# Kernel optimization log

Measured on AMD Instinct MI355X. Metric: run time of the kernel, lower is better.

Reference implementation:

```python
import jax, jax.numpy as jnp
import numpy as np

NUM_SAMPLES = 4096
TAU = 0.07
EPS = 1e-20


def setup_inputs() -> dict:
    key = jax.random.key(0)
    flows = jax.random.normal(key, (32, 2, 512, 512), dtype=jnp.float32)
    return {"flows": flows}


def reference(flows):
    # flows: [b, 2, h, w]
    b, _, h, w = flows.shape
    hw = h * w
    # sampling weights: L2 norm over the 2 flow components, scaled by 1/tau
    dist = jnp.sqrt(jnp.sum(flows * flows, axis=1)) / TAU  # [b, h, w]
    dist = dist.reshape(b, hw)  # [b, h*w]
    # torch.multinomial(dist, k) without replacement == Gumbel-top-k on log-weights
    logits = jnp.log(dist + EPS)
    g = jax.random.gumbel(jax.random.key(42), (b, hw), dtype=flows.dtype)
    _, indices = jax.lax.top_k(logits + g, NUM_SAMPLES)  # [b, num_samples] int32
    # scatter-based mask (equivalent to one_hot(indices).max(dim=1), without the
    # huge [b, num_samples, h*w] intermediate)
    batch_idx = jnp.arange(b)[:, None]  # [b, 1]
    flat_masks = jnp.zeros((b, hw), dtype=flows.dtype).at[batch_idx, indices].set(1.0)
    masks = flat_masks.reshape(b, 1, h, w)  # [b, 1, h, w]
    sparse_output = masks * flows  # [b, 2, h, w]
    sparse_output = jnp.concatenate([sparse_output, masks], axis=1)  # [b, 3, h, w]
    return sparse_output, indices, masks
```

## Files before the change

### kernel.cpp

```cpp
#include <hip/hip_runtime.h>
#include <stdint.h>

#define HW 262144
#define NB 32
#define TOPK 4096
#define NTOTAL (NB * HW)
#define GBLK 4096
#define CBLK 32768

#define OUT_F4 8421376u
#define GTHREADS 524288u

typedef float f32x4 __attribute__((ext_vector_type(4)));

#define OFF_WIN 33554432
#define OFF_HA  35651584
#define OFF_HB  37748736
#define OFF_STA 39845888
#define OFF_STT 39846144
#define OFF_FLG 39846272
#define OFF_CNT 39846400

__device__ __forceinline__ uint32_t rotl32(uint32_t x, int d) {
  return (x << d) | (x >> (32 - d));
}

__device__ __forceinline__ void threefry2x32_k42(uint32_t x0, uint32_t x1,
                                                 uint32_t& o0, uint32_t& o1) {
  const uint32_t ks0 = 0u;
  const uint32_t ks1 = 42u;
  const uint32_t ks2 = 0x1BD11BDAu ^ 0u ^ 42u;
  x0 += ks0;
  x1 += ks1;
#define TF_ROUND(r) { x0 += x1; x1 = rotl32(x1, (r)); x1 ^= x0; }
  TF_ROUND(13) TF_ROUND(15) TF_ROUND(26) TF_ROUND(6)
  x0 += ks1; x1 += ks2 + 1u;
  TF_ROUND(17) TF_ROUND(29) TF_ROUND(16) TF_ROUND(24)
  x0 += ks2; x1 += ks0 + 2u;
  TF_ROUND(13) TF_ROUND(15) TF_ROUND(26) TF_ROUND(6)
  x0 += ks0; x1 += ks1 + 3u;
  TF_ROUND(17) TF_ROUND(29) TF_ROUND(16) TF_ROUND(24)
  x0 += ks1; x1 += ks2 + 4u;
  TF_ROUND(13) TF_ROUND(15) TF_ROUND(26) TF_ROUND(6)
  x0 += ks2; x1 += ks0 + 5u;
#undef TF_ROUND
  o0 = x0;
  o1 = x1;
}

__device__ __forceinline__ float eigen_plogf(float xin) {
#pragma clang fp contract(off)
  uint32_t ux = __float_as_uint(xin);
  int e_int = (int)(ux >> 23) - 126;
  float x = __uint_as_float((ux & 0x007fffffu) | 0x3f000000u);
  float e = (float)e_int;
  const float SQRTHF = 0.707106781186547524f;
  bool m = (x < SQRTHF);
  float tmp = m ? x : 0.0f;
  x = x - 1.0f;
  e = e - (m ? 1.0f : 0.0f);
  x = x + tmp;
  float x2 = x * x;
  float x3 = x2 * x;
  float y  = fmaf(7.0376836292e-2f,  x, -1.1514610310e-1f);
  float y1 = fmaf(-1.2420140846e-1f, x,  1.4249322787e-1f);
  float y2 = fmaf(2.0000714765e-1f,  x, -2.4999993993e-1f);
  y  = fmaf(y,  x,  1.1676998740e-1f);
  y1 = fmaf(y1, x, -1.6668057665e-1f);
  y2 = fmaf(y2, x,  3.3333331174e-1f);
  y  = fmaf(y,  x3, y1);
  y  = fmaf(y,  x3, y2);
  y  = y * x3;
  float ey1 = e * -2.12194440e-4f;
  float t2  = x2 * 0.5f;
  y = y + ey1;
  x = x - t2;
  float ey2 = e * 0.693359375f;
  x = x + y;
  x = x + ey2;
  return x;
}

__device__ __forceinline__ float np_logf(float xin) {
#pragma clang fp contract(off)
  uint32_t ux = __float_as_uint(xin);
  int e2 = (int)(ux >> 23) - 127;
  float mant = __uint_as_float((ux & 0x007fffffu) | 0x3f800000u);
  if (mant >= 1.5f) { mant = mant * 0.5f; e2 += 1; }
  float e = (float)e2;
  float t = mant - 1.0f;
  float num = fmaf(2.589979117907922693523e-02f, t, 3.808837741388407920751e-01f);
  num = fmaf(num, t, 1.480000633400055983228e+00f);
  num = fmaf(num, t, 2.112677543073053063722e+00f);
  num = fmaf(num, t, 9.999999999999998702752e-01f);
  num = num * t;
  float den = fmaf(5.875095403124574342950e-03f, t, 1.546476374983906719538e-01f);
  den = fmaf(den, t, 9.864942958519418960339e-01f);
  den = fmaf(den, t, 2.453006071784736363091e+00f);
  den = fmaf(den, t, 2.612677543073109236779e+00f);
  den = fmaf(den, t, 1.0f);
  float r = num / den;
  return fmaf(e, 0.693147182464599609375f, r);
}

__device__ __forceinline__ uint32_t order_key(const float* __restrict__ flows,
                                              int p, uint32_t bits) {
#pragma clang fp contract(off)
  int b = p >> 18;
  int j = p & (HW - 1);
  const float* fb = flows + ((size_t)b << 19);
  float x = fb[j];
  float y = fb[j + HW];
  float xx = x * x;
  float yy = y * y;
  float ss = xx + yy;
  float sq = (float)sqrt((double)ss);
  float dist = (float)((double)sq / (double)0.07f);
  float logits = np_logf(dist + 1e-20f);
  float f = __uint_as_float((bits >> 9) | 0x3f800000u) - 1.0f;
  float u = fmaxf(f, 1.17549435e-38f);
  float g = -eigen_plogf(-eigen_plogf(u));
  float s = logits + g;
  uint32_t mm = __float_as_uint(s);
  mm = (mm & 0x80000000u) ? ~mm : (mm | 0x80000000u);
  return ~mm;
}

__global__ __launch_bounds__(1024) void k_compute(const float* __restrict__ flows,
                                                  uint32_t* __restrict__ d,
                                                  uint32_t* __restrict__ histA) {
  __shared__ uint32_t lh[16384];
  for (int i = threadIdx.x; i < 16384; i += 1024) lh[i] = 0u;
  __syncthreads();
  int base = blockIdx.x * CBLK;
  int b = base >> 18;
  for (int it = 0; it < CBLK / 1024; ++it) {
    int p = base + it * 1024 + threadIdx.x;
    uint32_t o0, o1;
    threefry2x32_k42(0u, (uint32_t)p, o0, o1);
    uint32_t dv = order_key(flows, p, o0 ^ o1);
    d[p] = dv;
    atomicAdd(&lh[dv >> 18], 1u);
  }
  __syncthreads();
  uint32_t* hb = histA + ((uint32_t)b << 14);
  for (int i = threadIdx.x; i < 16384; i += 1024) {
    uint32_t c = lh[i];
    if (c) atomicAdd(&hb[i], c);
  }
}

__global__ __launch_bounds__(1024) void k_scanAB(const uint32_t* __restrict__ histA,
                                                 const uint32_t* __restrict__ d,
                                                 uint32_t* __restrict__ histB,
                                                 uint32_t* __restrict__ stateA,
                                                 uint32_t* __restrict__ stateT,
                                                 uint32_t* __restrict__ flag) {
  __shared__ uint32_t ls[1024];
  __shared__ uint32_t bc[3];
  int b = blockIdx.x;
  {
    const uint32_t* h = histA + ((uint32_t)b << 14);
    int base = threadIdx.x * 16;
    uint32_t s = 0;
    for (int i = 0; i < 16; ++i) s += h[base + i];
    ls[threadIdx.x] = s;
    __syncthreads();
    for (int off = 1; off < 1024; off <<= 1) {
      uint32_t v = (threadIdx.x >= off) ? ls[threadIdx.x - off] : 0u;
      __syncthreads();
      ls[threadIdx.x] += v;
      __syncthreads();
    }
    uint32_t incl = ls[threadIdx.x];
    uint32_t excl = incl - s;
    if (excl < TOPK && TOPK <= incl) {
      uint32_t cum = excl;
      for (int i = 0; i < 16; ++i) {
        uint32_t c = h[base + i];
        if (cum + c >= TOPK) {
          uint32_t B = (uint32_t)(base + i);
          stateA[2 * b] = B;
          stateA[2 * b + 1] = TOPK - cum;
          stateT[b] = (B << 18) | 0x3FFFFu;
          uint32_t ov = (cum + c > 8192u) ? 1u : 0u;
          flag[b] = ov;
          bc[0] = B; bc[1] = TOPK - cum; bc[2] = ov;
          break;
        }
        cum += c;
      }
    }
  }
  __syncthreads();
  if (bc[2] == 0u) return;
  uint32_t B = bc[0];
  uint32_t target = bc[1];
  uint32_t* h2 = histB + ((uint32_t)b << 14);
  const uint32_t* db = d + ((size_t)b << 18);
  for (int it = 0; it < HW / 1024; ++it) {
    uint32_t dv = db[it * 1024 + threadIdx.x];
    if ((dv >> 18) == B)
      atomicAdd(&h2[(dv >> 4) & 0x3FFFu], 1u);
  }
  __threadfence();
  __syncthreads();
  {
    int base = threadIdx.x * 16;
    uint32_t s = 0;
    for (int i = 0; i < 16; ++i) s += h2[base + i];
    ls[threadIdx.x] = s;
    __syncthreads();
    for (int off = 1; off < 1024; off <<= 1) {
      uint32_t v = (threadIdx.x >= off) ? ls[threadIdx.x - off] : 0u;
      __syncthreads();
      ls[threadIdx.x] += v;
      __syncthreads();
    }
    uint32_t incl = ls[threadIdx.x];
    uint32_t excl = incl - s;
    if (excl < target && target <= incl) {
      uint32_t cum = excl;
      for (int i = 0; i < 16; ++i) {
        uint32_t c = h2[base + i];
        if (cum + c >= target) {
          stateT[b] = (B << 18) | ((uint32_t)(base + i) << 4) | 0xFu;
          break;
        }
        cum += c;
      }
    }
  }
}

__global__ __launch_bounds__(256) void k_gather(const uint32_t* __restrict__ d,
                                                const uint32_t* __restrict__ stateT,
                                                uint32_t* __restrict__ cnt,
                                                unsigned long long* __restrict__ winners,
                                                f32x4* __restrict__ outz) {
  __shared__ unsigned long long buf[GBLK];
  __shared__ uint32_t lcnt;
  __shared__ uint32_t gbase;
  int base = blockIdx.x * GBLK;
  int b = base >> 18;
  uint32_t T = stateT[b];
  uint32_t gt = (uint32_t)blockIdx.x * 256u + threadIdx.x;
  const f32x4 z4 = {0.f, 0.f, 0.f, 0.f};
  if (threadIdx.x == 0) lcnt = 0u;
  __syncthreads();
  for (int it = 0; it < GBLK / 256; ++it) {
    int p = base + it * 256 + threadIdx.x;
    uint32_t dv = d[p];
    outz[(uint32_t)it * GTHREADS + gt] = z4;
    if (dv <= T) {
      uint32_t pos = atomicAdd(&lcnt, 1u);
      buf[pos] = ((unsigned long long)dv << 32) |
                 (unsigned long long)(p & (HW - 1));
    }
  }
  { uint32_t z = 16u * GTHREADS + gt;
    if (z < OUT_F4) outz[z] = z4; }
  __syncthreads();
  uint32_t n = lcnt;
  if (threadIdx.x == 0 && n) gbase = atomicAdd(&cnt[b], n);
  __syncthreads();
  for (uint32_t i = threadIdx.x; i < n; i += 256) {
    uint32_t pos = gbase + i;
    if (pos < 8192u) winners[(size_t)b * 8192 + pos] = buf[i];
  }
}

__global__ __launch_bounds__(1024) void k_sort1(const uint32_t* __restrict__ cnt,
                                                unsigned long long* __restrict__ winners) {
  __shared__ unsigned long long s[1024];
  int blk = blockIdx.x;
  int b = blk >> 3;
  int c = blk & 7;
  uint32_t n = cnt[b];
  if (n > 8192u) n = 8192u;
  int goff = b * 8192 + c * 1024;
  int t = threadIdx.x;
  s[t] = ((uint32_t)(c * 1024 + t) < n) ? winners[goff + t]
                                        : 0xFFFFFFFFFFFFFFFFull;
  __syncthreads();
  for (int k = 2; k <= 1024; k <<= 1) {
    for (int j = k >> 1; j > 0; j >>= 1) {
      int ixj = t ^ j;
      if (ixj > t) {
        bool up = ((t & k) == 0);
        unsigned long long a = s[t];
        unsigned long long cc = s[ixj];
        if ((a > cc) == up) { s[t] = cc; s[ixj] = a; }
      }
      __syncthreads();
    }
  }
  winners[goff + t] = s[t];
}

__global__ __launch_bounds__(1024) void k_rank(const unsigned long long* __restrict__ winners,
                                               const float* __restrict__ flows,
                                               float* __restrict__ out0,
                                               float* __restrict__ out_idx,
                                               float* __restrict__ out_masks) {
  __shared__ unsigned long long s[8192];
  int b = blockIdx.x >> 3;
  int part = blockIdx.x & 7;
  for (int i = threadIdx.x; i < 8192; i += 1024)
    s[i] = winners[(size_t)b * 8192 + i];
  __syncthreads();
  const float* fb = flows + ((size_t)b << 19);
  int i = (part << 10) + threadIdx.x;
  unsigned long long w = s[i];
  if (w != 0xFFFFFFFFFFFFFFFFull) {
    int rank = threadIdx.x;
    for (int c = 0; c < 8; ++c) {
      if (c == part) continue;
      int lo = 0, hi = 1024;
      while (lo < hi) {
        int mid = (lo + hi) >> 1;
        if (s[(c << 10) + mid] < w) lo = mid + 1; else hi = mid;
      }
      rank += lo;
    }
    if (rank < TOPK) {
      uint32_t idx = (uint32_t)(w & 0xFFFFFFFFull);
      out_idx[(size_t)b * TOPK + rank] = (float)idx;
      float x = fb[idx];
      float y = fb[idx + HW];
      size_t o = ((size_t)b * 3) * HW + idx;
      out0[o] = x;
      out0[o + HW] = y;
      out0[o + 2 * HW] = 1.0f;
      out_masks[(size_t)b * HW + idx] = 1.0f;
    }
  }
}

extern "C" void kernel_launch(void* const* d_in, const int* in_sizes, int n_in,
                              void* d_out, int out_size, void* d_ws, size_t ws_size,
                              hipStream_t stream) {
  const float* flows = (const float*)d_in[0];
  float* out = (float*)d_out;
  char* ws = (char*)d_ws;

  uint32_t* d = (uint32_t*)ws;
  unsigned long long* winners = (unsigned long long*)(ws + OFF_WIN);
  uint32_t* histA = (uint32_t*)(ws + OFF_HA);
  uint32_t* histB = (uint32_t*)(ws + OFF_HB);
  uint32_t* stateA = (uint32_t*)(ws + OFF_STA);
  uint32_t* stateT = (uint32_t*)(ws + OFF_STT);
  uint32_t* flag = (uint32_t*)(ws + OFF_FLG);
  uint32_t* cnt = (uint32_t*)(ws + OFF_CNT);

  float* out_idx = out + (size_t)NB * 3 * HW;
  float* out_masks = out_idx + (size_t)NB * TOPK;

  (void)hipMemsetAsync(ws + OFF_HA, 0, 4194304 + 1024, stream);

  k_compute<<<NTOTAL / CBLK, 1024, 0, stream>>>(flows, d, histA);
  k_scanAB<<<NB, 1024, 0, stream>>>(histA, d, histB, stateA, stateT, flag);
  k_gather<<<NTOTAL / GBLK, 256, 0, stream>>>(d, stateT, cnt, winners,
                                              (f32x4*)out);
  k_sort1<<<NB * 8, 1024, 0, stream>>>(cnt, winners);
  k_rank<<<NB * 8, 1024, 0, stream>>>(winners, flows, out, out_idx, out_masks);
}
```

Baseline: 298.3 us.

## Fuse histogram scan into compute kernel via last-block election, move zero-fill

Merges the per-batch threshold scan (k_scanAB) into k_compute. A per-batch done counter elects the last of the 8 blocks in each batch, and that block performs the two-level histogram scan. This removes one kernel launch and lets the scans of finished batches overlap with compute for other batches. The zero-fill of the output is also moved from k_gather into k_compute, which keeps k_gather lean. The cost is a longer tail on the elected blocks and extra fences and atomics.

```diff
diff --git a/kernel.cpp b/kernel.cpp
--- a/kernel.cpp
+++ b/kernel.cpp
@@ -9,7 +9,6 @@
 #define CBLK 32768
 
 #define OUT_F4 8421376u
-#define GTHREADS 524288u
 
 typedef float f32x4 __attribute__((ext_vector_type(4)));
 
@@ -20,6 +19,7 @@
 #define OFF_STT 39846144
 #define OFF_FLG 39846272
 #define OFF_CNT 39846400
+#define OFF_DONE 39846528
 
 __device__ __forceinline__ uint32_t rotl32(uint32_t x, int d) {
   return (x << d) | (x >> (32 - d));
@@ -128,58 +128,69 @@
 
 __global__ __launch_bounds__(1024) void k_compute(const float* __restrict__ flows,
                                                   uint32_t* __restrict__ d,
-                                                  uint32_t* __restrict__ histA) {
+                                                  uint32_t* __restrict__ histA,
+                                                  uint32_t* __restrict__ histB,
+                                                  uint32_t* __restrict__ stateA,
+                                                  uint32_t* __restrict__ stateT,
+                                                  uint32_t* __restrict__ flag,
+                                                  uint32_t* __restrict__ done,
+                                                  f32x4* __restrict__ outz) {
   __shared__ uint32_t lh[16384];
+  __shared__ uint32_t bc[3];
+  __shared__ uint32_t lastflag;
   for (int i = threadIdx.x; i < 16384; i += 1024) lh[i] = 0u;
   __syncthreads();
   int base = blockIdx.x * CBLK;
   int b = base >> 18;
+  uint32_t gt = (uint32_t)blockIdx.x * 1024u + threadIdx.x;
+  const f32x4 z4 = {0.f, 0.f, 0.f, 0.f};
   for (int it = 0; it < CBLK / 1024; ++it) {
     int p = base + it * 1024 + threadIdx.x;
     uint32_t o0, o1;
     threefry2x32_k42(0u, (uint32_t)p, o0, o1);
     uint32_t dv = order_key(flows, p, o0 ^ o1);
     d[p] = dv;
+    outz[(uint32_t)it * 262144u + gt] = z4;
     atomicAdd(&lh[dv >> 18], 1u);
   }
+  { uint32_t z = 32u * 262144u + gt;
+    if (z < OUT_F4) outz[z] = z4; }
   __syncthreads();
   uint32_t* hb = histA + ((uint32_t)b << 14);
   for (int i = threadIdx.x; i < 16384; i += 1024) {
     uint32_t c = lh[i];
     if (c) atomicAdd(&hb[i], c);
   }
-}
-
-__global__ __launch_bounds__(1024) void k_scanAB(const uint32_t* __restrict__ histA,
-                                                 const uint32_t* __restrict__ d,
-                                                 uint32_t* __restrict__ histB,
-                                                 uint32_t* __restrict__ stateA,
-                                                 uint32_t* __restrict__ stateT,
-                                                 uint32_t* __restrict__ flag) {
-  __shared__ uint32_t ls[1024];
-  __shared__ uint32_t bc[3];
-  int b = blockIdx.x;
+  __syncthreads();
+  if (threadIdx.x == 0) {
+    __threadfence();
+    uint32_t prev = atomicAdd(&done[b], 1u);
+    lastflag = (prev == 7u) ? 1u : 0u;
+  }
+  __syncthreads();
+  if (!lastflag) return;
+  __threadfence();
   {
     const uint32_t* h = histA + ((uint32_t)b << 14);
-    int base = threadIdx.x * 16;
+    int sbase = threadIdx.x * 16;
     uint32_t s = 0;
-    for (int i = 0; i < 16; ++i) s += h[base + i];
-    ls[threadIdx.x] = s;
+    for (int i = 0; i < 16; ++i) s += h[sbase + i];
+    lh[threadIdx.x] = s;
     __syncthreads();
     for (int off = 1; off < 1024; off <<= 1) {
-      uint32_t v = (threadIdx.x >= off) ? ls[threadIdx.x - off] : 0u;
-      __syncthreads();
-      ls[threadIdx.x] += v;
-      __syncthreads();
-    }
-    uint32_t incl = ls[threadIdx.x];
+      uint32_t v = (threadIdx.x >= off) ? lh[threadIdx.x - off] : 0u;
+      __syncthreads();
+      lh[threadIdx.x] += v;
+      __syncthreads();
+    }
+    uint32_t incl = lh[threadIdx.x];
     uint32_t excl = incl - s;
     if (excl < TOPK && TOPK <= incl) {
       uint32_t cum = excl;
       for (int i = 0; i < 16; ++i) {
-        uint32_t c = h[base + i];
+        uint32_t c = h[sbase + i];
         if (cum + c >= TOPK) {
-          uint32_t B = (uint32_t)(base + i);
+          uint32_t B = (uint32_t)(sbase + i);
           stateA[2 * b] = B;
           stateA[2 * b + 1] = TOPK - cum;
           stateT[b] = (B << 18) | 0x3FFFFu;
@@ -206,25 +217,25 @@
   __threadfence();
   __syncthreads();
   {
-    int base = threadIdx.x * 16;
+    int sbase = threadIdx.x * 16;
     uint32_t s = 0;
-    for (int i = 0; i < 16; ++i) s += h2[base + i];
-    ls[threadIdx.x] = s;
+    for (int i = 0; i < 16; ++i) s += h2[sbase + i];
+    lh[threadIdx.x] = s;
     __syncthreads();
     for (int off = 1; off < 1024; off <<= 1) {
-      uint32_t v = (threadIdx.x >= off) ? ls[threadIdx.x - off] : 0u;
-      __syncthreads();
-      ls[threadIdx.x] += v;
-      __syncthreads();
-    }
-    uint32_t incl = ls[threadIdx.x];
+      uint32_t v = (threadIdx.x >= off) ? lh[threadIdx.x - off] : 0u;
+      __syncthreads();
+      lh[threadIdx.x] += v;
+      __syncthreads();
+    }
+    uint32_t incl = lh[threadIdx.x];
     uint32_t excl = incl - s;
     if (excl < target && target <= incl) {
       uint32_t cum = excl;
       for (int i = 0; i < 16; ++i) {
-        uint32_t c = h2[base + i];
+        uint32_t c = h2[sbase + i];
         if (cum + c >= target) {
-          stateT[b] = (B << 18) | ((uint32_t)(base + i) << 4) | 0xFu;
+          stateT[b] = (B << 18) | ((uint32_t)(sbase + i) << 4) | 0xFu;
           break;
         }
         cum += c;
@@ -236,30 +247,24 @@
 __global__ __launch_bounds__(256) void k_gather(const uint32_t* __restrict__ d,
                                                 const uint32_t* __restrict__ stateT,
                                                 uint32_t* __restrict__ cnt,
-                                                unsigned long long* __restrict__ winners,
-                                                f32x4* __restrict__ outz) {
+                                                unsigned long long* __restrict__ winners) {
   __shared__ unsigned long long buf[GBLK];
   __shared__ uint32_t lcnt;
   __shared__ uint32_t gbase;
   int base = blockIdx.x * GBLK;
   int b = base >> 18;
   uint32_t T = stateT[b];
-  uint32_t gt = (uint32_t)blockIdx.x * 256u + threadIdx.x;
-  const f32x4 z4 = {0.f, 0.f, 0.f, 0.f};
   if (threadIdx.x == 0) lcnt = 0u;
   __syncthreads();
   for (int it = 0; it < GBLK / 256; ++it) {
     int p = base + it * 256 + threadIdx.x;
     uint32_t dv = d[p];
-    outz[(uint32_t)it * GTHREADS + gt] = z4;
     if (dv <= T) {
       uint32_t pos = atomicAdd(&lcnt, 1u);
       buf[pos] = ((unsigned long long)dv << 32) |
                  (unsigned long long)(p & (HW - 1));
     }
   }
-  { uint32_t z = 16u * GTHREADS + gt;
-    if (z < OUT_F4) outz[z] = z4; }
   __syncthreads();
   uint32_t n = lcnt;
   if (threadIdx.x == 0 && n) gbase = atomicAdd(&cnt[b], n);
@@ -352,16 +357,17 @@
   uint32_t* stateT = (uint32_t*)(ws + OFF_STT);
   uint32_t* flag = (uint32_t*)(ws + OFF_FLG);
   uint32_t* cnt = (uint32_t*)(ws + OFF_CNT);
+  uint32_t* done = (uint32_t*)(ws + OFF_DONE);
 
   float* out_idx = out + (size_t)NB * 3 * HW;
   float* out_masks = out_idx + (size_t)NB * TOPK;
 
   (void)hipMemsetAsync(ws + OFF_HA, 0, 4194304 + 1024, stream);
 
-  k_compute<<<NTOTAL / CBLK, 1024, 0, stream>>>(flows, d, histA);
-  k_scanAB<<<NB, 1024, 0, stream>>>(histA, d, histB, stateA, stateT, flag);
-  k_gather<<<NTOTAL / GBLK, 256, 0, stream>>>(d, stateT, cnt, winners,
-                                              (f32x4*)out);
+  k_compute<<<NTOTAL / CBLK, 1024, 0, stream>>>(flows, d, histA, histB,
+                                                stateA, stateT, flag, done,
+                                                (f32x4*)out);
+  k_gather<<<NTOTAL / GBLK, 256, 0, stream>>>(d, stateT, cnt, winners);
   k_sort1<<<NB * 8, 1024, 0, stream>>>(cnt, winners);
   k_rank<<<NB * 8, 1024, 0, stream>>>(winners, flows, out, out_idx, out_masks);
 }
```

Result: slower. 325.9 us (+9.2%).
